# Optimization experiments

Hardware: AMD Instinct MI355X
Metric: run time of the kernel (lower is better)

Reference implementation:

```python
import jax, jax.numpy as jnp
import numpy as np

N_USERS, N_MOVIES, M, K = 100000, 20000, 8, 32
B = 524288

def setup_inputs() -> dict:
    key = jax.random.key(0)
    k1, k2, k3, k4 = jax.random.split(key, 4)
    edge = jax.random.randint(k1, (B, 2), 0, 20000, dtype=jnp.int64) if jax.config.jax_enable_x64 else jax.random.randint(k1, (B, 2), 0, 20000, dtype=jnp.int32)
    std = 1.0 / K
    taste_emb = jax.random.normal(k2, (N_USERS, M * K), dtype=jnp.float32) * std
    attn_emb = jax.random.normal(k3, (N_USERS, M * K), dtype=jnp.float32) * std
    movie_emb = jax.random.normal(k4, (N_MOVIES, K), dtype=jnp.float32) * std
    user_bias = jnp.zeros((N_USERS, 1), dtype=jnp.float32)
    movie_bias = jnp.zeros((N_MOVIES, 1), dtype=jnp.float32)
    return {"edge": edge, "taste_emb": taste_emb, "attn_emb": attn_emb,
            "movie_emb": movie_emb, "user_bias": user_bias, "movie_bias": movie_bias}

def reference(edge, taste_emb, attn_emb, movie_emb, user_bias, movie_bias):
    u = edge[:, 0]
    v = edge[:, 1]
    A = attn_emb[u].reshape(-1, M, K)   # [B, m, k]
    U = taste_emb[u].reshape(-1, M, K)  # [B, m, k]
    e = movie_emb[v]                    # [B, k]
    logits = jnp.einsum('bmk,bk->bm', A, e)          # bmm(A, e) -> [B, m]
    att = jax.nn.softmax(logits, axis=1)             # softmax over m tastes
    scores = jnp.einsum('bmk,bk->bm', U, e)          # bmm(U, e) -> [B, m]
    y_hat = jnp.sum(scores * att, axis=1) + movie_bias[v, 0] + user_bias[u, 0]
    return y_hat  # [B]
```

## Files before the change

kernel.cpp:

```cpp
#include <hip/hip_runtime.h>


#define MOT_CAP     64
#define MOT_OVF_CAP 4096

using half8 = __attribute__((ext_vector_type(8))) _Float16;
using f32x4 = __attribute__((ext_vector_type(4))) float;

__global__ void mot_zero_kernel(int4* __restrict__ p, int n4) {
    const int i = blockIdx.x * 256 + (int)threadIdx.x;
    if (i < n4) p[i] = make_int4(0, 0, 0, 0);
}

__device__ __forceinline__ float mot_score_div(const float* __restrict__ Ar,
                                               const float* __restrict__ Tr,
                                               const float4* __restrict__ Ep) {
    float4 ek[8];
    #pragma unroll
    for (int k4 = 0; k4 < 8; ++k4) ek[k4] = Ep[k4];
    float num = 0.f, den = 0.f;
    #pragma unroll
    for (int m = 0; m < 8; ++m) {
        float l = 0.f, s = 0.f;
        #pragma unroll
        for (int k4 = 0; k4 < 8; ++k4) {
            const float4 a = *(const float4*)(Ar + m * 32 + k4 * 4);
            const float4 t = *(const float4*)(Tr + m * 32 + k4 * 4);
            const float4 e = ek[k4];
            l = fmaf(a.x, e.x, l); l = fmaf(a.y, e.y, l);
            l = fmaf(a.z, e.z, l); l = fmaf(a.w, e.w, l);
            s = fmaf(t.x, e.x, s); s = fmaf(t.y, e.y, s);
            s = fmaf(t.z, e.z, s); s = fmaf(t.w, e.w, s);
        }
        const float ex = __expf(l);
        den += ex;
        num = fmaf(ex, s, num);
    }
    return num / den;
}

__global__ void mot_scatter_kernel(const int4* __restrict__ edge2,
                                   int* __restrict__ cnt,
                                   int* __restrict__ ovfMeta,
                                   int* __restrict__ ovf,
                                   int2* __restrict__ sve,
                                   int nPairs, int nEdges) {
    const int i = blockIdx.x * 256 + (int)threadIdx.x;
    if (i < nPairs) {
        const int4 q = edge2[i];
        int pos = atomicAdd(&cnt[q.x], 1);
        if (pos < MOT_CAP) sve[(size_t)q.x * MOT_CAP + pos] = make_int2(q.y, 2 * i);
        else { int o = atomicAdd(ovfMeta, 1); if (o < MOT_OVF_CAP) ovf[o] = 2 * i; }
        pos = atomicAdd(&cnt[q.z], 1);
        if (pos < MOT_CAP) sve[(size_t)q.z * MOT_CAP + pos] = make_int2(q.w, 2 * i + 1);
        else { int o = atomicAdd(ovfMeta, 1); if (o < MOT_OVF_CAP) ovf[o] = 2 * i + 1; }
    } else if (i == nPairs && (nEdges & 1)) {
        const int2 e = ((const int2*)edge2)[nEdges - 1];
        int pos = atomicAdd(&cnt[e.x], 1);
        if (pos < MOT_CAP) sve[(size_t)e.x * MOT_CAP + pos] = make_int2(e.y, nEdges - 1);
        else { int o = atomicAdd(ovfMeta, 1); if (o < MOT_OVF_CAP) ovf[o] = nEdges - 1; }
    }
}

__device__ __forceinline__ half8 mot_load_afrag(const float* __restrict__ attn_emb,
                                                const float* __restrict__ taste_emb,
                                                int u, int row, int k0) {
    const float* rowp = (row < 8)
        ? attn_emb  + (size_t)u * 256 + row * 32 + k0
        : taste_emb + (size_t)u * 256 + (row - 8) * 32 + k0;
    const float4 r0 = *(const float4*)rowp;
    const float4 r1 = *(const float4*)(rowp + 4);
    half8 af;
    af[0] = (_Float16)r0.x; af[1] = (_Float16)r0.y;
    af[2] = (_Float16)r0.z; af[3] = (_Float16)r0.w;
    af[4] = (_Float16)r1.x; af[5] = (_Float16)r1.y;
    af[6] = (_Float16)r1.z; af[7] = (_Float16)r1.w;
    return af;
}

__global__ __launch_bounds__(256, 6) void mot_mfma2_kernel(
    const int2* __restrict__ edge,
    const float* __restrict__ taste_emb,
    const float* __restrict__ attn_emb,
    const float4* __restrict__ movie_emb,
    const float* __restrict__ user_bias,
    const float* __restrict__ movie_bias,
    const int* __restrict__ cnt,
    const int2* __restrict__ sve,
    const int* __restrict__ ovfMeta,
    const int* __restrict__ ovf,
    float* __restrict__ out,
    int nUsers, int mainBlocks)
{
    const int tid  = (int)threadIdx.x;
    const int lane = tid & 63;

    if ((int)blockIdx.x < mainBlocks) {
        const int u0 = ((int)blockIdx.x * 4 + (tid >> 6)) * 2;
        const int u1 = u0 + 1;
        if (u0 >= nUsers) return;

        const int row = lane & 15;
        const int kq  = lane >> 4;
        const int k0  = kq * 8;
        const int hi  = kq & 1;

        int n0 = cnt[u0]; n0 = n0 > MOT_CAP ? MOT_CAP : n0;
        int n1 = (u1 < nUsers) ? cnt[u1] : 0; n1 = n1 > MOT_CAP ? MOT_CAP : n1;
        const half8 af0 = mot_load_afrag(attn_emb, taste_emb, u0, row, k0);
        const half8 af1 = mot_load_afrag(attn_emb, taste_emb, u1, row, k0);
        const float ub0 = user_bias[u0];
        const float ub1 = user_bias[u1];
        const int2* __restrict__ b0 = sve + (size_t)u0 * MOT_CAP;
        const int2* __restrict__ b1 = sve + (size_t)u1 * MOT_CAP;

        int t0 = 0, t1 = 0;
        while (t0 < n0 || t1 < n1) {
            const bool d0 = t0 < n0, d1 = t1 < n1;

            int2 ve0 = make_int2(0, -1), ve1 = make_int2(0, -1);
            half8 bf0 = {}, bf1 = {};
            bool val0 = false, val1 = false;
            if (d0) {
                const int ei = t0 + row;
                val0 = ei < n0;
                if (val0) {
                    ve0 = b0[ei];
                    const float4* __restrict__ Ep = movie_emb + (size_t)ve0.x * 8;
                    const float4 e0 = Ep[kq * 2], e1 = Ep[kq * 2 + 1];
                    bf0[0] = (_Float16)e0.x; bf0[1] = (_Float16)e0.y;
                    bf0[2] = (_Float16)e0.z; bf0[3] = (_Float16)e0.w;
                    bf0[4] = (_Float16)e1.x; bf0[5] = (_Float16)e1.y;
                    bf0[6] = (_Float16)e1.z; bf0[7] = (_Float16)e1.w;
                }
            }
            if (d1) {
                const int ei = t1 + row;
                val1 = ei < n1;
                if (val1) {
                    ve1 = b1[ei];
                    const float4* __restrict__ Ep = movie_emb + (size_t)ve1.x * 8;
                    const float4 e0 = Ep[kq * 2], e1 = Ep[kq * 2 + 1];
                    bf1[0] = (_Float16)e0.x; bf1[1] = (_Float16)e0.y;
                    bf1[2] = (_Float16)e0.z; bf1[3] = (_Float16)e0.w;
                    bf1[4] = (_Float16)e1.x; bf1[5] = (_Float16)e1.y;
                    bf1[6] = (_Float16)e1.z; bf1[7] = (_Float16)e1.w;
                }
            }

            #pragma unroll
            for (int g = 0; g < 2; ++g) {
                const bool dg = g ? d1 : d0;
                if (!dg) continue;
                const half8 af = g ? af1 : af0;
                const half8 bf = g ? bf1 : bf0;
                const bool val = g ? val1 : val0;
                const int2 ve = g ? ve1 : ve0;
                const float ub = g ? ub1 : ub0;

                f32x4 c = {0.f, 0.f, 0.f, 0.f};
                c = __builtin_amdgcn_mfma_f32_16x16x32_f16(af, bf, c, 0, 0, 0);

                const float o0 = __shfl_xor(c[0], 16);
                const float o1 = __shfl_xor(c[1], 16);
                const float o2 = __shfl_xor(c[2], 16);
                const float o3 = __shfl_xor(c[3], 16);
                float v0 = hi ? o0 : c[0], v1 = hi ? o1 : c[1];
                float v2 = hi ? o2 : c[2], v3 = hi ? o3 : c[3];
                float v4 = hi ? c[0] : o0, v5 = hi ? c[1] : o1;
                float v6 = hi ? c[2] : o2, v7 = hi ? c[3] : o3;
                const float w0 = __shfl_xor(v0, 32), w1 = __shfl_xor(v1, 32);
                const float w2 = __shfl_xor(v2, 32), w3 = __shfl_xor(v3, 32);
                const float w4 = __shfl_xor(v4, 32), w5 = __shfl_xor(v5, 32);
                const float w6 = __shfl_xor(v6, 32), w7 = __shfl_xor(v7, 32);

                if (kq == 0 && val) {
                    float den = 0.f, num = 0.f;
                    const float e0x = __expf(v0); den += e0x; num = fmaf(e0x, w0, num);
                    const float e1x = __expf(v1); den += e1x; num = fmaf(e1x, w1, num);
                    const float e2x = __expf(v2); den += e2x; num = fmaf(e2x, w2, num);
                    const float e3x = __expf(v3); den += e3x; num = fmaf(e3x, w3, num);
                    const float e4x = __expf(v4); den += e4x; num = fmaf(e4x, w4, num);
                    const float e5x = __expf(v5); den += e5x; num = fmaf(e5x, w5, num);
                    const float e6x = __expf(v6); den += e6x; num = fmaf(e6x, w6, num);
                    const float e7x = __expf(v7); den += e7x; num = fmaf(e7x, w7, num);
                    out[ve.y] = num * __builtin_amdgcn_rcpf(den) + ub + movie_bias[ve.x];
                }
            }
            t0 += 16; t1 += 16;
        }
    } else {
        int oc = ovfMeta[0];
        if (oc > MOT_OVF_CAP) oc = MOT_OVF_CAP;
        const int oi = ((int)blockIdx.x - mainBlocks) * 256 + tid;
        if (oi < oc) {
            const int eid = ovf[oi];
            const int2 ed = edge[eid];
            out[eid] = mot_score_div(attn_emb  + (size_t)ed.x * 256,
                                     taste_emb + (size_t)ed.x * 256,
                                     movie_emb + (size_t)ed.y * 8)
                       + user_bias[ed.x] + movie_bias[ed.y];
        }
    }
}

__global__ __launch_bounds__(256, 4) void mot_flat_kernel(
    const int2* __restrict__ edge,
    const float4* __restrict__ taste_emb,
    const float4* __restrict__ attn_emb,
    const float4* __restrict__ movie_emb,
    const float* __restrict__ user_bias,
    const float* __restrict__ movie_bias,
    float* __restrict__ out,
    int nEdges)
{
    const int tid  = blockIdx.x * 256 + (int)threadIdx.x;
    const int eid  = tid >> 5;
    const int s    = tid & 31;
    if (eid >= nEdges) return;
    const int2 ed = edge[eid];
    const int u = ed.x, v = ed.y;
    const float4* Ap = attn_emb  + (size_t)u * 64;
    const float4* Tp = taste_emb + (size_t)u * 64;
    const float4* Ep = movie_emb + (size_t)v * 8;
    const float4 a0 = Ap[2 * s], a1 = Ap[2 * s + 1];
    const float4 t0 = Tp[2 * s], t1 = Tp[2 * s + 1];
    const int c = s & 3;
    const float4 e0 = Ep[2 * c], e1 = Ep[2 * c + 1];
    float lp = a0.x*e0.x + a0.y*e0.y + a0.z*e0.z + a0.w*e0.w
             + a1.x*e1.x + a1.y*e1.y + a1.z*e1.z + a1.w*e1.w;
    float sp = t0.x*e0.x + t0.y*e0.y + t0.z*e0.z + t0.w*e0.w
             + t1.x*e1.x + t1.y*e1.y + t1.z*e1.z + t1.w*e1.w;
    lp += __shfl_xor(lp, 1); lp += __shfl_xor(lp, 2);
    sp += __shfl_xor(sp, 1); sp += __shfl_xor(sp, 2);
    const float ex = __expf(lp);
    float den = ex, num = ex * sp;
    den += __shfl_xor(den, 4);  num += __shfl_xor(num, 4);
    den += __shfl_xor(den, 8);  num += __shfl_xor(num, 8);
    den += __shfl_xor(den, 16); num += __shfl_xor(num, 16);
    if (s == 0) out[eid] = num / den + user_bias[u] + movie_bias[v];
}

extern "C" void kernel_launch(void* const* d_in, const int* in_sizes, int n_in,
                              void* d_out, int out_size, void* d_ws, size_t ws_size,
                              hipStream_t stream) {
    const int2*   edge       = (const int2*)d_in[0];
    const float*  taste_emb  = (const float*)d_in[1];
    const float*  attn_emb   = (const float*)d_in[2];
    const float*  movie_emb  = (const float*)d_in[3];
    const float*  user_bias  = (const float*)d_in[4];
    const float*  movie_bias = (const float*)d_in[5];
    float*        out        = (float*)d_out;

    const int nEdges = in_sizes[0] / 2;
    const int NB     = in_sizes[3] / 32;

    auto align256 = [](size_t x) { return (x + 255) & ~(size_t)255; };
    char* ws = (char*)d_ws;

    const size_t o_cnt  = 0;
    const size_t o_meta = align256((size_t)NB * 4);
    const size_t o_ovf  = o_meta + 256;
    const size_t o_sve  = align256(o_ovf + (size_t)MOT_OVF_CAP * 4);
    const size_t need   = o_sve + (size_t)NB * MOT_CAP * 8;

    if (ws_size < need) {
        const int blocks = (nEdges * 32 + 255) / 256;
        mot_flat_kernel<<<blocks, 256, 0, stream>>>(
            edge, (const float4*)taste_emb, (const float4*)attn_emb,
            (const float4*)movie_emb, user_bias, movie_bias, out, nEdges);
        return;
    }

    int*  cnt     = (int*)(ws + o_cnt);
    int*  ovfMeta = (int*)(ws + o_meta);
    int*  ovf     = (int*)(ws + o_ovf);
    int2* sve     = (int2*)(ws + o_sve);

    const int n4 = (int)(o_ovf / 16);
    mot_zero_kernel<<<(n4 + 255) / 256, 256, 0, stream>>>((int4*)ws, n4);

    const int nPairs  = nEdges / 2;
    const int sblocks = (nPairs + 1 + 255) / 256;
    mot_scatter_kernel<<<sblocks, 256, 0, stream>>>(
        (const int4*)edge, cnt, ovfMeta, ovf, sve, nPairs, nEdges);

    const int mainBlocks = (NB + 7) / 8;
    const int ovfBlocks  = MOT_OVF_CAP / 256;
    mot_mfma2_kernel<<<mainBlocks + ovfBlocks, 256, 0, stream>>>(
        edge, taste_emb, attn_emb, (const float4*)movie_emb,
        user_bias, movie_bias, cnt, sve, ovfMeta, ovf, out, NB, mainBlocks);
}
```

Baseline: 66.23 us.

## Prefetch all user edge tiles up front and simplify softmax reduction shuffles

Replaces the per-16-edge while loop with a fully unrolled four-tile structure. All of a user's bucket entries and their movie embedding fragments are issued up front so the gathers overlap, rather than serialising load then MFMA per tile. The softmax combine now has each lane exponentiate its own four logits and reduce num/den with one xor-16 shuffle pair, replacing the select-heavy eight-way shuffle. Costs are higher register pressure (occupancy hint lowered from 6 to 4) and loads of unused sve slots clamped to index 0. nMovies is passed as NB, which is only safe because the edge indices stay below 20000.

```diff
diff --git a/kernel.cpp b/kernel.cpp
--- a/kernel.cpp
+++ b/kernel.cpp
@@ -78,7 +78,7 @@
     return af;
 }
 
-__global__ __launch_bounds__(256, 6) void mot_mfma2_kernel(
+__global__ __launch_bounds__(256, 4) void mot_mfma4_kernel(
     const int2* __restrict__ edge,
     const float* __restrict__ taste_emb,
     const float* __restrict__ attn_emb,
@@ -90,7 +90,7 @@
     const int* __restrict__ ovfMeta,
     const int* __restrict__ ovf,
     float* __restrict__ out,
-    int nUsers, int mainBlocks)
+    int nUsers, int nMovies, int mainBlocks)
 {
     const int tid  = (int)threadIdx.x;
     const int lane = tid & 63;
@@ -103,91 +103,82 @@
         const int row = lane & 15;
         const int kq  = lane >> 4;
         const int k0  = kq * 8;
-        const int hi  = kq & 1;
+
+        const int2* __restrict__ b0 = sve + (size_t)u0 * MOT_CAP;
+        const int2* __restrict__ b1 = sve + (size_t)u1 * MOT_CAP;
+
+        int2 ve0[4], ve1[4];
+        #pragma unroll
+        for (int T = 0; T < 4; ++T) ve0[T] = b0[T * 16 + row];
+        #pragma unroll
+        for (int T = 0; T < 4; ++T) ve1[T] = b1[T * 16 + row];
 
         int n0 = cnt[u0]; n0 = n0 > MOT_CAP ? MOT_CAP : n0;
         int n1 = (u1 < nUsers) ? cnt[u1] : 0; n1 = n1 > MOT_CAP ? MOT_CAP : n1;
+        const float ub0 = user_bias[u0];
+        const float ub1 = user_bias[u1];
+
         const half8 af0 = mot_load_afrag(attn_emb, taste_emb, u0, row, k0);
         const half8 af1 = mot_load_afrag(attn_emb, taste_emb, u1, row, k0);
-        const float ub0 = user_bias[u0];
-        const float ub1 = user_bias[u1];
-        const int2* __restrict__ b0 = sve + (size_t)u0 * MOT_CAP;
-        const int2* __restrict__ b1 = sve + (size_t)u1 * MOT_CAP;
-
-        int t0 = 0, t1 = 0;
-        while (t0 < n0 || t1 < n1) {
-            const bool d0 = t0 < n0, d1 = t1 < n1;
-
-            int2 ve0 = make_int2(0, -1), ve1 = make_int2(0, -1);
-            half8 bf0 = {}, bf1 = {};
-            bool val0 = false, val1 = false;
-            if (d0) {
-                const int ei = t0 + row;
-                val0 = ei < n0;
-                if (val0) {
-                    ve0 = b0[ei];
-                    const float4* __restrict__ Ep = movie_emb + (size_t)ve0.x * 8;
-                    const float4 e0 = Ep[kq * 2], e1 = Ep[kq * 2 + 1];
-                    bf0[0] = (_Float16)e0.x; bf0[1] = (_Float16)e0.y;
-                    bf0[2] = (_Float16)e0.z; bf0[3] = (_Float16)e0.w;
-                    bf0[4] = (_Float16)e1.x; bf0[5] = (_Float16)e1.y;
-                    bf0[6] = (_Float16)e1.z; bf0[7] = (_Float16)e1.w;
+
+        half8 bf0[4], bf1[4];
+        #pragma unroll
+        for (int g2 = 0; g2 < 2; ++g2) {
+            const int2* ve = g2 ? ve1 : ve0;
+            half8* bf = g2 ? bf1 : bf0;
+            #pragma unroll
+            for (int T = 0; T < 4; ++T) {
+                const int vx = ((unsigned)ve[T].x < (unsigned)nMovies) ? ve[T].x : 0;
+                const float4* __restrict__ Ep = movie_emb + (size_t)vx * 8;
+                const float4 e0 = Ep[kq * 2], e1 = Ep[kq * 2 + 1];
+                half8 b;
+                b[0] = (_Float16)e0.x; b[1] = (_Float16)e0.y;
+                b[2] = (_Float16)e0.z; b[3] = (_Float16)e0.w;
+                b[4] = (_Float16)e1.x; b[5] = (_Float16)e1.y;
+                b[6] = (_Float16)e1.z; b[7] = (_Float16)e1.w;
+                bf[T] = b;
+            }
+        }
+
+        #pragma unroll
+        for (int T = 0; T < 4; ++T) {
+            #pragma unroll
+            for (int g = 0; g < 2; ++g) {
+                const int n = g ? n1 : n0;
+                if (T * 16 >= n) continue;
+                const half8 af = g ? af1 : af0;
+                const half8 bf = g ? bf0[0] : bf0[0];
+                (void)bf;
+                const half8 bfx = g ? bf1[T] : bf0[T];
+                const int2 ve = g ? ve1[T] : ve0[T];
+                const float ub = g ? ub1 : ub0;
+
+                f32x4 c = {0.f, 0.f, 0.f, 0.f};
+                c = __builtin_amdgcn_mfma_f32_16x16x32_f16(af, bfx, c, 0, 0, 0);
+
+                const float s0 = __shfl_xor(c[0], 32);
+                const float s1 = __shfl_xor(c[1], 32);
+                const float s2 = __shfl_xor(c[2], 32);
+                const float s3 = __shfl_xor(c[3], 32);
+                const float e0x = __expf(c[0]);
+                const float e1x = __expf(c[1]);
+                const float e2x = __expf(c[2]);
+                const float e3x = __expf(c[3]);
+                float den = e0x + e1x + e2x + e3x;
+                float num = e0x * s0;
+                num = fmaf(e1x, s1, num);
+                num = fmaf(e2x, s2, num);
+                num = fmaf(e3x, s3, num);
+                den += __shfl_xor(den, 16);
+                num += __shfl_xor(num, 16);
+
+                if (kq == 0) {
+                    const int ei = T * 16 + row;
+                    if (ei < n)
+                        out[ve.y] = num * __builtin_amdgcn_rcpf(den) + ub
+                                    + movie_bias[ve.x];
                 }
             }
-            if (d1) {
-                const int ei = t1 + row;
-                val1 = ei < n1;
-                if (val1) {
-                    ve1 = b1[ei];
-                    const float4* __restrict__ Ep = movie_emb + (size_t)ve1.x * 8;
-                    const float4 e0 = Ep[kq * 2], e1 = Ep[kq * 2 + 1];
-                    bf1[0] = (_Float16)e0.x; bf1[1] = (_Float16)e0.y;
-                    bf1[2] = (_Float16)e0.z; bf1[3] = (_Float16)e0.w;
-                    bf1[4] = (_Float16)e1.x; bf1[5] = (_Float16)e1.y;
-                    bf1[6] = (_Float16)e1.z; bf1[7] = (_Float16)e1.w;
-                }
-            }
-
-            #pragma unroll
-            for (int g = 0; g < 2; ++g) {
-                const bool dg = g ? d1 : d0;
-                if (!dg) continue;
-                const half8 af = g ? af1 : af0;
-                const half8 bf = g ? bf1 : bf0;
-                const bool val = g ? val1 : val0;
-                const int2 ve = g ? ve1 : ve0;
-                const float ub = g ? ub1 : ub0;
-
-                f32x4 c = {0.f, 0.f, 0.f, 0.f};
-                c = __builtin_amdgcn_mfma_f32_16x16x32_f16(af, bf, c, 0, 0, 0);
-
-                const float o0 = __shfl_xor(c[0], 16);
-                const float o1 = __shfl_xor(c[1], 16);
-                const float o2 = __shfl_xor(c[2], 16);
-                const float o3 = __shfl_xor(c[3], 16);
-                float v0 = hi ? o0 : c[0], v1 = hi ? o1 : c[1];
-                float v2 = hi ? o2 : c[2], v3 = hi ? o3 : c[3];
-                float v4 = hi ? c[0] : o0, v5 = hi ? c[1] : o1;
-                float v6 = hi ? c[2] : o2, v7 = hi ? c[3] : o3;
-                const float w0 = __shfl_xor(v0, 32), w1 = __shfl_xor(v1, 32);
-                const float w2 = __shfl_xor(v2, 32), w3 = __shfl_xor(v3, 32);
-                const float w4 = __shfl_xor(v4, 32), w5 = __shfl_xor(v5, 32);
-                const float w6 = __shfl_xor(v6, 32), w7 = __shfl_xor(v7, 32);
-
-                if (kq == 0 && val) {
-                    float den = 0.f, num = 0.f;
-                    const float e0x = __expf(v0); den += e0x; num = fmaf(e0x, w0, num);
-                    const float e1x = __expf(v1); den += e1x; num = fmaf(e1x, w1, num);
-                    const float e2x = __expf(v2); den += e2x; num = fmaf(e2x, w2, num);
-                    const float e3x = __expf(v3); den += e3x; num = fmaf(e3x, w3, num);
-                    const float e4x = __expf(v4); den += e4x; num = fmaf(e4x, w4, num);
-                    const float e5x = __expf(v5); den += e5x; num = fmaf(e5x, w5, num);
-                    const float e6x = __expf(v6); den += e6x; num = fmaf(e6x, w6, num);
-                    const float e7x = __expf(v7); den += e7x; num = fmaf(e7x, w7, num);
-                    out[ve.y] = num * __builtin_amdgcn_rcpf(den) + ub + movie_bias[ve.x];
-                }
-            }
-            t0 += 16; t1 += 16;
         }
     } else {
         int oc = ovfMeta[0];
@@ -287,7 +278,7 @@
 
     const int mainBlocks = (NB + 7) / 8;
     const int ovfBlocks  = MOT_OVF_CAP / 256;
-    mot_mfma2_kernel<<<mainBlocks + ovfBlocks, 256, 0, stream>>>(
+    mot_mfma4_kernel<<<mainBlocks + ovfBlocks, 256, 0, stream>>>(
         edge, taste_emb, attn_emb, (const float4*)movie_emb,
-        user_bias, movie_bias, cnt, sve, ovfMeta, ovf, out, NB, mainBlocks);
-}
+        user_bias, movie_bias, cnt, sve, ovfMeta, ovf, out, NB, NB, mainBlocks);
+}
```

After: 65.75 us. About the same (-0.7%).
